# Kernel optimization log

Hardware: AMD Instinct MI355X
Metric: run time of the kernel (lower is better)

## Reference

```python
import jax, jax.numpy as jnp
import numpy as np

B, D, LD, LP = 8, 192, 128, 1024
FC = [1024, 1024, 512]
NC = 2


def setup_inputs() -> dict:
    key = jax.random.key(0)
    ks = jax.random.split(key, 18)
    s = 0.05  # small init scale for numerical sanity
    inp = {
        "drug_conv": jax.random.normal(ks[0], (B, D, LD), jnp.float32),
        "protein_conv": jax.random.normal(ks[1], (B, D, LP), jnp.float32),
        "Wd": jax.random.normal(ks[2], (D, D), jnp.float32) * s,
        "bd": jax.random.normal(ks[3], (D,), jnp.float32) * s,
        "Wp": jax.random.normal(ks[4], (D, D), jnp.float32) * s,
        "bp": jax.random.normal(ks[5], (D,), jnp.float32) * s,
        "Wa": jax.random.normal(ks[6], (D, D), jnp.float32) * s,
        "ba": jax.random.normal(ks[7], (D,), jnp.float32) * s,
        "W1": jax.random.normal(ks[8], (FC[0], 2 * D), jnp.float32) * s,
        "b1": jax.random.normal(ks[9], (FC[0],), jnp.float32) * s,
        "W2": jax.random.normal(ks[10], (FC[1], FC[0]), jnp.float32) * s,
        "b2": jax.random.normal(ks[11], (FC[1],), jnp.float32) * s,
        "W3": jax.random.normal(ks[12], (FC[2], FC[1]), jnp.float32) * s,
        "b3": jax.random.normal(ks[13], (FC[2],), jnp.float32) * s,
        "Wo": jax.random.normal(ks[14], (NC, FC[2]), jnp.float32) * s,
        "bo": jax.random.normal(ks[15], (NC,), jnp.float32) * s,
    }
    return inp


def reference(drug_conv, protein_conv, Wd, bd, Wp, bp, Wa, ba,
              W1, b1, W2, b2, W3, b3, Wo, bo):
    # drug_conv: (B, D, Ld); protein_conv: (B, D, Lp). Torch Linear: y = x @ W.T + b
    d_att = jnp.einsum('bdl,ed->ble', drug_conv, Wd) + bd      # (B, Ld, D)
    p_att = jnp.einsum('bdl,ed->ble', protein_conv, Wp) + bp   # (B, Lp, D)
    # broadcast additive cross-attention: (B, Ld, Lp, D)
    h = jax.nn.relu(d_att[:, :, None, :] + p_att[:, None, :, :])
    A = jnp.einsum('blpd,ed->blpe', h, Wa) + ba                # (B, Ld, Lp, D)
    comp_att = jax.nn.sigmoid(jnp.mean(A, axis=2))             # (B, Ld, D)
    prot_att = jax.nn.sigmoid(jnp.mean(A, axis=1))             # (B, Lp, D)
    # gated residual: x*0.5 + x*att  (att permuted back to (B, D, L))
    drug = drug_conv * (0.5 + jnp.transpose(comp_att, (0, 2, 1)))
    prot = protein_conv * (0.5 + jnp.transpose(prot_att, (0, 2, 1)))
    # MaxPool1d over full sequence length == max along last axis
    drug_pooled = jnp.max(drug, axis=2)                        # (B, D)
    prot_pooled = jnp.max(prot, axis=2)                        # (B, D)
    pair = jnp.concatenate([drug_pooled, prot_pooled], axis=1) # (B, 2D)
    lrelu = lambda x: jax.nn.leaky_relu(x, 0.01)
    h1 = lrelu(pair @ W1.T + b1)
    h2 = lrelu(h1 @ W2.T + b2)
    h3 = lrelu(h2 @ W3.T + b3)
    return h3 @ Wo.T + bo                                      # (B, num_classes)
```

## Files before the change

kernel.cpp:

```cpp
#include <hip/hip_runtime.h>
#include <math.h>

#define BB 8
#define DD 192
#define LLD 128
#define LLP 1024
#define FC1 1024
#define FC2 1024
#define FC3 512
#define NCLS 2
#define LT 8

__device__ __forceinline__ void atomicMaxFloat(float* addr, float value) {
    if (value >= 0.f)
        atomicMax((int*)addr, __float_as_int(value));
    else
        atomicMin((unsigned int*)addr, __float_as_uint(value));
}

__global__ void proj_both_kernel(const float* __restrict__ drug,
                                 const float* __restrict__ prot,
                                 const float* __restrict__ Wd,
                                 const float* __restrict__ bdv,
                                 const float* __restrict__ Wp,
                                 const float* __restrict__ bpv,
                                 float* __restrict__ d_att,
                                 float* __restrict__ p_att) {
    int blk = blockIdx.x;
    const float *x, *W, *bias;
    float* y;
    int L, b, l0;
    if (blk < BB * (LLD / LT)) {
        x = drug; W = Wd; bias = bdv; y = d_att; L = LLD;
        b = blk >> 4; l0 = (blk & 15) * LT;
    } else {
        int idx = blk - BB * (LLD / LT);
        x = prot; W = Wp; bias = bpv; y = p_att; L = LLP;
        b = idx >> 7; l0 = (idx & 127) * LT;
    }
    int tid = threadIdx.x;

    __shared__ float xs[LT][DD + 4];

    const float* xbase = x + (size_t)b * DD * L + l0;
#pragma unroll
    for (int k = 0; k < LT; ++k) {
        int idx = tid + k * DD;
        int d = idx >> 3;
        int j = idx & (LT - 1);
        xs[j][d] = xbase[(size_t)d * L + j];
    }
    __syncthreads();

    const int e = tid;
    const float be = bias[e];
    float acc[LT];
#pragma unroll
    for (int j = 0; j < LT; ++j) acc[j] = be;

    const float4* Wr4 = (const float4*)(W + (size_t)e * DD);
#pragma unroll 2
    for (int d4 = 0; d4 < DD / 4; ++d4) {
        float4 w = Wr4[d4];
#pragma unroll
        for (int j = 0; j < LT; ++j) {
            float4 h = *(const float4*)&xs[j][d4 * 4];
            acc[j] = fmaf(h.x, w.x, acc[j]);
            acc[j] = fmaf(h.y, w.y, acc[j]);
            acc[j] = fmaf(h.z, w.z, acc[j]);
            acc[j] = fmaf(h.w, w.w, acc[j]);
        }
    }

    float* ybase = y + ((size_t)b * L + l0) * DD;
#pragma unroll
    for (int j = 0; j < LT; ++j)
        ybase[(size_t)j * DD + e] = acc[j];
}

__global__ void cross_sort_kernel(const float* __restrict__ da,
                                  const float* __restrict__ pa,
                                  float* __restrict__ Hd_t,
                                  float* __restrict__ Hp_t,
                                  float* __restrict__ pair) {
    int blk = blockIdx.x;
    int b = blk / (DD / 2);
    int dp = blk - b * (DD / 2);
    int d0 = dp * 2;
    int tid = threadIdx.x;
    int wave = tid >> 6, lane = tid & 63;

    __shared__ float skey[2][LLD];
    __shared__ float sufs[2][LLD + 1];
    __shared__ int   cnt[2][LLD + 1];
    __shared__ float val[2][LLD + 1];

    float s0 = 0.f, s1 = 0.f;
    int i0 = 0, i1 = 0;

    if (wave < 2) {
        const int a = wave;
        const float* base = da + (size_t)b * LLD * DD + d0 + a;
        s0 = base[(size_t)lane * DD];
        s1 = base[(size_t)(lane + 64) * DD];
        i0 = lane; i1 = lane + 64;

        for (int k = 2; k <= LLD; k <<= 1) {
            for (int j = k >> 1; j > 0; j >>= 1) {
                if (j == 64) {
                    if (s0 > s1) {
                        float tk = s0; s0 = s1; s1 = tk;
                        int ti = i0; i0 = i1; i1 = ti;
                    }
                } else {
                    {
                        float pk = __shfl_xor(s0, j);
                        int   pi = __shfl_xor(i0, j);
                        bool keep_min = (((lane & k) == 0) == ((lane & j) == 0));
                        bool take = keep_min ? (pk < s0) : (pk > s0);
                        if (take) { s0 = pk; i0 = pi; }
                    }
                    {
                        int e = lane | 64;
                        float pk = __shfl_xor(s1, j);
                        int   pi = __shfl_xor(i1, j);
                        bool keep_min = (((e & k) == 0) == ((e & j) == 0));
                        bool take = keep_min ? (pk < s1) : (pk > s1);
                        if (take) { s1 = pk; i1 = pi; }
                    }
                }
            }
        }

        float t1 = s1;
#pragma unroll
        for (int off = 1; off < 64; off <<= 1) {
            int src = lane + off;
            float v = __shfl(t1, src & 63);
            t1 += (src < 64) ? v : 0.f;
        }
        float tot1 = __shfl(t1, 0);
        float t0 = s0;
#pragma unroll
        for (int off = 1; off < 64; off <<= 1) {
            int src = lane + off;
            float v = __shfl(t0, src & 63);
            t0 += (src < 64) ? v : 0.f;
        }

        skey[a][lane] = s0;
        skey[a][lane + 64] = s1;
        sufs[a][lane] = t0 + tot1;
        sufs[a][lane + 64] = t1;
        if (lane == 0) sufs[a][LLD] = 0.f;
    } else if (wave == 2) {
        for (int i = lane; i < 2 * (LLD + 1); i += 64) ((int*)cnt)[i] = 0;
        if (lane < 4) {
            int side = lane >> 1;
            pair[b * 2 * DD + side * DD + d0 + (lane & 1)] = -INFINITY;
        }
    } else {
        for (int i = lane; i < 2 * (LLD + 1); i += 64) ((float*)val)[i] = 0.f;
    }
    __syncthreads();

    {
        int d_i = tid & 1, prow = tid >> 1;
        float* hprow = Hp_t + ((size_t)b * DD + d0 + d_i) * LLP;
        const float* qbase = pa + (size_t)b * LLP * DD + d0 + d_i;
#pragma unroll
        for (int batch = 0; batch < LLP / 128; ++batch) {
            int p = batch * 128 + prow;
            float q = qbase[(size_t)p * DD];
            float nq = -q;
            int pos = 0;
#pragma unroll
            for (int st = LLD; st > 0; st >>= 1) {
                int np = pos + st;
                if (np <= LLD && skey[d_i][np - 1] <= nq) pos = np;
            }
            hprow[p] = ((float)(LLD - pos) * q + sufs[d_i][pos]) * (1.0f / LLD);
            atomicAdd(&cnt[d_i][pos], 1);
            atomicAdd(&val[d_i][pos], q);
        }
    }
    __syncthreads();

    if (wave < 2) {
        const int a = wave;
        int   c0 = cnt[a][lane], c1 = cnt[a][lane + 64];
        float v0 = val[a][lane], v1 = val[a][lane + 64];
#pragma unroll
        for (int off = 1; off < 64; off <<= 1) {
            int src = lane - off;
            int   cu = __shfl(c0, src & 63);
            float vu = __shfl(v0, src & 63);
            if (src >= 0) { c0 += cu; v0 += vu; }
        }
        int   ct0 = __shfl(c0, 63);
        float vt0 = __shfl(v0, 63);
#pragma unroll
        for (int off = 1; off < 64; off <<= 1) {
            int src = lane - off;
            int   cu = __shfl(c1, src & 63);
            float vu = __shfl(v1, src & 63);
            if (src >= 0) { c1 += cu; v1 += vu; }
        }
        c1 += ct0; v1 += vt0;

        float* hdrow = Hd_t + ((size_t)b * DD + d0 + a) * LLD;
        hdrow[i0] = (s0 * (float)c0 + v0) * (1.0f / LLP);
        hdrow[i1] = (s1 * (float)c1 + v1) * (1.0f / LLP);
    }
}

__global__ void gemm_sig_pool_kernel(const float* __restrict__ Hd_t,
                                     const float* __restrict__ Hp_t,
                                     const float* __restrict__ Wa,
                                     const float* __restrict__ ba,
                                     const float* __restrict__ drug,
                                     const float* __restrict__ prot,
                                     float* __restrict__ pair) {
    int blk = blockIdx.x;
    const float* Ht;
    const float* xsrc;
    int L, b, l0, side;
    if (blk < BB * (LLD / LT)) {
        b = blk >> 4; l0 = (blk & 15) * LT;
        Ht = Hd_t; xsrc = drug; L = LLD; side = 0;
    } else {
        int idx = blk - BB * (LLD / LT);
        b = idx >> 7; l0 = (idx & 127) * LT;
        Ht = Hp_t; xsrc = prot; L = LLP; side = 1;
    }
    int tid = threadIdx.x;

    __shared__ float hs[LT][DD + 4];

    const float* hrow = Ht + ((size_t)b * DD + tid) * L + l0;
#pragma unroll
    for (int j = 0; j < LT; ++j) hs[j][tid] = hrow[j];
    __syncthreads();

    const int e = tid;
    const float bias = ba[e];
    float acc[LT];
#pragma unroll
    for (int j = 0; j < LT; ++j) acc[j] = bias;

    const float4* Wr4 = (const float4*)(Wa + (size_t)e * DD);
#pragma unroll 2
    for (int d4 = 0; d4 < DD / 4; ++d4) {
        float4 w = Wr4[d4];
#pragma unroll
        for (int j = 0; j < LT; ++j) {
            float4 h = *(const float4*)&hs[j][d4 * 4];
            acc[j] = fmaf(h.x, w.x, acc[j]);
            acc[j] = fmaf(h.y, w.y, acc[j]);
            acc[j] = fmaf(h.z, w.z, acc[j]);
            acc[j] = fmaf(h.w, w.w, acc[j]);
        }
    }

    const float* xrow = xsrc + ((size_t)b * DD + e) * L + l0;
    float4 x0 = *(const float4*)&xrow[0];
    float4 x1 = *(const float4*)&xrow[4];
    float xv[LT] = {x0.x, x0.y, x0.z, x0.w, x1.x, x1.y, x1.z, x1.w};
    float m = -INFINITY;
#pragma unroll
    for (int j = 0; j < LT; ++j) {
        float gate = 0.5f + 1.0f / (1.0f + __expf(-acc[j]));
        m = fmaxf(m, xv[j] * gate);
    }
    atomicMaxFloat(&pair[b * 2 * DD + side * DD + e], m);
}

__global__ void fc_wave_kernel(const float* __restrict__ x,
                               const float* __restrict__ W,
                               const float* __restrict__ bias,
                               float* __restrict__ y,
                               int K, int N, int leaky) {
    int gtid = blockIdx.x * blockDim.x + threadIdx.x;
    int wid = gtid >> 6;
    int lane = gtid & 63;
    if (wid >= BB * N) return;
    int b = wid / N;
    int j = wid - b * N;
    const float4* xr = (const float4*)(x + (size_t)b * K);
    const float4* Wr = (const float4*)(W + (size_t)j * K);
    int K4 = K >> 2;
    float s = 0.f;
    for (int k = lane; k < K4; k += 64) {
        float4 xv = xr[k];
        float4 wv = Wr[k];
        s = fmaf(xv.x, wv.x, s);
        s = fmaf(xv.y, wv.y, s);
        s = fmaf(xv.z, wv.z, s);
        s = fmaf(xv.w, wv.w, s);
    }
#pragma unroll
    for (int off = 32; off > 0; off >>= 1) s += __shfl_xor(s, off);
    if (lane == 0) {
        float acc = s + bias[j];
        if (leaky) acc = (acc > 0.f) ? acc : 0.01f * acc;
        y[wid] = acc;
    }
}

extern "C" void kernel_launch(void* const* d_in, const int* in_sizes, int n_in,
                              void* d_out, int out_size, void* d_ws, size_t ws_size,
                              hipStream_t stream) {
    const float* drug = (const float*)d_in[0];
    const float* prot = (const float*)d_in[1];
    const float* Wd = (const float*)d_in[2];
    const float* bd = (const float*)d_in[3];
    const float* Wp = (const float*)d_in[4];
    const float* bp = (const float*)d_in[5];
    const float* Wa = (const float*)d_in[6];
    const float* ba = (const float*)d_in[7];
    const float* W1 = (const float*)d_in[8];
    const float* b1 = (const float*)d_in[9];
    const float* W2 = (const float*)d_in[10];
    const float* b2 = (const float*)d_in[11];
    const float* W3 = (const float*)d_in[12];
    const float* b3 = (const float*)d_in[13];
    const float* Wo = (const float*)d_in[14];
    const float* bo = (const float*)d_in[15];
    float* out = (float*)d_out;

    float* ws = (float*)d_ws;
    const size_t n_datt = (size_t)BB * LLD * DD;
    const size_t n_patt = (size_t)BB * LLP * DD;
    float* d_att  = ws;
    float* p_att  = d_att + n_datt;
    float* Hd_t   = p_att + n_patt;
    float* Hp_t   = Hd_t + n_datt;
    float* pair   = Hp_t + n_patt;
    float* h1     = pair + (size_t)BB * 2 * DD;
    float* h2     = h1 + (size_t)BB * FC1;
    float* h3     = h2 + (size_t)BB * FC2;

    proj_both_kernel<<<BB * (LLD / LT) + BB * (LLP / LT), DD, 0, stream>>>(
        drug, prot, Wd, bd, Wp, bp, d_att, p_att);

    cross_sort_kernel<<<BB * (DD / 2), 256, 0, stream>>>(d_att, p_att, Hd_t, Hp_t, pair);

    gemm_sig_pool_kernel<<<BB * (LLD / LT) + BB * (LLP / LT), DD, 0, stream>>>(
        Hd_t, Hp_t, Wa, ba, drug, prot, pair);

    fc_wave_kernel<<<(BB * FC1 * 64) / 256, 256, 0, stream>>>(pair, W1, b1, h1, 2 * DD, FC1, 1);
    fc_wave_kernel<<<(BB * FC2 * 64) / 256, 256, 0, stream>>>(h1, W2, b2, h2, FC1, FC2, 1);
    fc_wave_kernel<<<(BB * FC3 * 64) / 256, 256, 0, stream>>>(h2, W3, b3, h3, FC2, FC3, 1);
    fc_wave_kernel<<<(BB * NCLS * 64 + 255) / 256, 256, 0, stream>>>(h3, Wo, bo, out, FC3, NCLS, 0);
}
```

Baseline: 94.60 us.

## Store projections transposed and fuse final FC layer via last-block counter

The projection kernel now writes d_att and p_att in (B, D, L) layout using float4 stores. This makes the cross-sort kernel's per-channel reads contiguous instead of strided by D. Separately, the FC3 and output layers are merged into one kernel: the last block to finish, detected with an atomic counter that the projection kernel resets, computes the tiny output GEMV. This removes one launch at the cost of a threadfence and atomic in every block.

```diff
diff --git a/kernel.cpp b/kernel.cpp
--- a/kernel.cpp
+++ b/kernel.cpp
@@ -12,10 +12,8 @@
 #define LT 8
 
 __device__ __forceinline__ void atomicMaxFloat(float* addr, float value) {
-    if (value >= 0.f)
-        atomicMax((int*)addr, __float_as_int(value));
-    else
-        atomicMin((unsigned int*)addr, __float_as_uint(value));
+    if (value >= 0.f) atomicMax((int*)addr, __float_as_int(value));
+    else atomicMin((unsigned int*)addr, __float_as_uint(value));
 }
 
 __global__ void proj_both_kernel(const float* __restrict__ drug,
@@ -24,21 +22,24 @@
                                  const float* __restrict__ bdv,
                                  const float* __restrict__ Wp,
                                  const float* __restrict__ bpv,
-                                 float* __restrict__ d_att,
-                                 float* __restrict__ p_att) {
+                                 float* __restrict__ d_att_t,
+                                 float* __restrict__ p_att_t,
+                                 int* __restrict__ counter) {
     int blk = blockIdx.x;
+    int tid = threadIdx.x;
+    if (blk == 0 && tid == 0) *counter = 0;
+
     const float *x, *W, *bias;
     float* y;
     int L, b, l0;
     if (blk < BB * (LLD / LT)) {
-        x = drug; W = Wd; bias = bdv; y = d_att; L = LLD;
+        x = drug; W = Wd; bias = bdv; y = d_att_t; L = LLD;
         b = blk >> 4; l0 = (blk & 15) * LT;
     } else {
         int idx = blk - BB * (LLD / LT);
-        x = prot; W = Wp; bias = bpv; y = p_att; L = LLP;
+        x = prot; W = Wp; bias = bpv; y = p_att_t; L = LLP;
         b = idx >> 7; l0 = (idx & 127) * LT;
     }
-    int tid = threadIdx.x;
 
     __shared__ float xs[LT][DD + 4];
 
@@ -72,14 +73,13 @@
         }
     }
 
-    float* ybase = y + ((size_t)b * L + l0) * DD;
-#pragma unroll
-    for (int j = 0; j < LT; ++j)
-        ybase[(size_t)j * DD + e] = acc[j];
-}
-
-__global__ void cross_sort_kernel(const float* __restrict__ da,
-                                  const float* __restrict__ pa,
+    float* ybase = y + ((size_t)b * DD + e) * L + l0;
+    *(float4*)&ybase[0] = make_float4(acc[0], acc[1], acc[2], acc[3]);
+    *(float4*)&ybase[4] = make_float4(acc[4], acc[5], acc[6], acc[7]);
+}
+
+__global__ void cross_sort_kernel(const float* __restrict__ da_t,
+                                  const float* __restrict__ pa_t,
                                   float* __restrict__ Hd_t,
                                   float* __restrict__ Hp_t,
                                   float* __restrict__ pair) {
@@ -100,9 +100,9 @@
 
     if (wave < 2) {
         const int a = wave;
-        const float* base = da + (size_t)b * LLD * DD + d0 + a;
-        s0 = base[(size_t)lane * DD];
-        s1 = base[(size_t)(lane + 64) * DD];
+        const float* base = da_t + ((size_t)b * DD + d0 + a) * LLD;
+        s0 = base[lane];
+        s1 = base[lane + 64];
         i0 = lane; i1 = lane + 64;
 
         for (int k = 2; k <= LLD; k <<= 1) {
@@ -167,11 +167,11 @@
     {
         int d_i = tid & 1, prow = tid >> 1;
         float* hprow = Hp_t + ((size_t)b * DD + d0 + d_i) * LLP;
-        const float* qbase = pa + (size_t)b * LLP * DD + d0 + d_i;
+        const float* qbase = pa_t + ((size_t)b * DD + d0 + d_i) * LLP;
 #pragma unroll
         for (int batch = 0; batch < LLP / 128; ++batch) {
             int p = batch * 128 + prow;
-            float q = qbase[(size_t)p * DD];
+            float q = qbase[p];
             float nq = -q;
             int pos = 0;
 #pragma unroll
@@ -307,6 +307,64 @@
     }
 }
 
+__global__ void fc3_out_kernel(const float* __restrict__ x,
+                               const float* __restrict__ W3,
+                               const float* __restrict__ b3,
+                               float* __restrict__ h3,
+                               const float* __restrict__ Wo,
+                               const float* __restrict__ bo,
+                               float* __restrict__ out,
+                               int* __restrict__ counter) {
+    int gtid = blockIdx.x * blockDim.x + threadIdx.x;
+    int wid = gtid >> 6;
+    int lane = gtid & 63;
+    int b = wid / FC3;
+    int j = wid - b * FC3;
+    {
+        const float4* xr = (const float4*)(x + (size_t)b * FC2);
+        const float4* Wr = (const float4*)(W3 + (size_t)j * FC2);
+        float s = 0.f;
+        for (int k = lane; k < FC2 / 4; k += 64) {
+            float4 xv = xr[k], wv = Wr[k];
+            s = fmaf(xv.x, wv.x, s);
+            s = fmaf(xv.y, wv.y, s);
+            s = fmaf(xv.z, wv.z, s);
+            s = fmaf(xv.w, wv.w, s);
+        }
+#pragma unroll
+        for (int off = 32; off > 0; off >>= 1) s += __shfl_xor(s, off);
+        if (lane == 0) {
+            float acc = s + b3[j];
+            h3[wid] = (acc > 0.f) ? acc : 0.01f * acc;
+        }
+    }
+    __threadfence();
+    __shared__ int is_last;
+    if (threadIdx.x == 0)
+        is_last = (atomicAdd(counter, 1) == (int)gridDim.x - 1);
+    __syncthreads();
+    if (is_last) {
+        __threadfence();
+        int w4 = threadIdx.x >> 6;
+        for (int o = w4; o < BB * NCLS; o += 4) {
+            int b2 = o / NCLS, j2 = o - b2 * NCLS;
+            const float4* xr = (const float4*)(h3 + (size_t)b2 * FC3);
+            const float4* Wr = (const float4*)(Wo + (size_t)j2 * FC3);
+            float s = 0.f;
+            for (int k = lane; k < FC3 / 4; k += 64) {
+                float4 xv = xr[k], wv = Wr[k];
+                s = fmaf(xv.x, wv.x, s);
+                s = fmaf(xv.y, wv.y, s);
+                s = fmaf(xv.z, wv.z, s);
+                s = fmaf(xv.w, wv.w, s);
+            }
+#pragma unroll
+            for (int off = 32; off > 0; off >>= 1) s += __shfl_xor(s, off);
+            if (lane == 0) out[o] = s + bo[j2];
+        }
+    }
+}
+
 extern "C" void kernel_launch(void* const* d_in, const int* in_sizes, int n_in,
                               void* d_out, int out_size, void* d_ws, size_t ws_size,
                               hipStream_t stream) {
@@ -331,25 +389,26 @@
     float* ws = (float*)d_ws;
     const size_t n_datt = (size_t)BB * LLD * DD;
     const size_t n_patt = (size_t)BB * LLP * DD;
-    float* d_att  = ws;
-    float* p_att  = d_att + n_datt;
-    float* Hd_t   = p_att + n_patt;
-    float* Hp_t   = Hd_t + n_datt;
-    float* pair   = Hp_t + n_patt;
-    float* h1     = pair + (size_t)BB * 2 * DD;
-    float* h2     = h1 + (size_t)BB * FC1;
-    float* h3     = h2 + (size_t)BB * FC2;
+    float* d_att_t = ws;
+    float* p_att_t = d_att_t + n_datt;
+    float* Hd_t    = p_att_t + n_patt;
+    float* Hp_t    = Hd_t + n_datt;
+    float* pair    = Hp_t + n_patt;
+    float* h1      = pair + (size_t)BB * 2 * DD;
+    float* h2      = h1 + (size_t)BB * FC1;
+    float* h3      = h2 + (size_t)BB * FC2;
+    int*   counter = (int*)(h3 + (size_t)BB * FC3);
 
     proj_both_kernel<<<BB * (LLD / LT) + BB * (LLP / LT), DD, 0, stream>>>(
-        drug, prot, Wd, bd, Wp, bp, d_att, p_att);
-
-    cross_sort_kernel<<<BB * (DD / 2), 256, 0, stream>>>(d_att, p_att, Hd_t, Hp_t, pair);
+        drug, prot, Wd, bd, Wp, bp, d_att_t, p_att_t, counter);
+
+    cross_sort_kernel<<<BB * (DD / 2), 256, 0, stream>>>(
+        d_att_t, p_att_t, Hd_t, Hp_t, pair);
 
     gemm_sig_pool_kernel<<<BB * (LLD / LT) + BB * (LLP / LT), DD, 0, stream>>>(
         Hd_t, Hp_t, Wa, ba, drug, prot, pair);
 
     fc_wave_kernel<<<(BB * FC1 * 64) / 256, 256, 0, stream>>>(pair, W1, b1, h1, 2 * DD, FC1, 1);
     fc_wave_kernel<<<(BB * FC2 * 64) / 256, 256, 0, stream>>>(h1, W2, b2, h2, FC1, FC2, 1);
-    fc_wave_kernel<<<(BB * FC3 * 64) / 256, 256, 0, stream>>>(h2, W3, b3, h3, FC2, FC3, 1);
-    fc_wave_kernel<<<(BB * NCLS * 64 + 255) / 256, 256, 0, stream>>>(h3, Wo, bo, out, FC3, NCLS, 0);
-}
+    fc3_out_kernel<<<(BB * FC3 * 64) / 256, 256, 0, stream>>>(h2, W3, b3, h3, Wo, bo, out, counter);
+}
```

After: 159.8 us. +68.9%, slower.
